# Optimization experiments

Hardware: AMD Instinct MI355X
Metric: run time of the kernel (lower is better)

The kernel has to match this reference:

```python
import jax, jax.numpy as jnp
import numpy as np

B, T, D = 4, 2048, 1024
H = 16
HD = D // H  # 64
MAX_POS = 4096


def setup_inputs() -> dict:
    key = jax.random.key(0)
    k1, k2, k3, k4 = jax.random.split(key, 4)
    x = jax.random.normal(k1, (B, T, D), dtype=jnp.float32)
    position_ids = jnp.sort(jax.random.randint(k2, (B, T), 0, MAX_POS), axis=-1)
    Wqkv = jax.random.normal(k3, (D, 3 * D), dtype=jnp.float32) * (D ** -0.5)
    Wout = jax.random.normal(k4, (D, D), dtype=jnp.float32) * (D ** -0.5)
    return {"x": x, "position_ids": position_ids, "Wqkv": Wqkv, "Wout": Wout}


def reference(x, position_ids, Wqkv, Wout):
    Bv, Tv, Dv = x.shape
    # qkv projection: (B,T,3,H,HD)
    qkv = (x @ Wqkv).reshape(Bv, Tv, 3, H, HD)
    q, k, v = jnp.moveaxis(qkv, 2, 0)  # each (B,T,H,HD)
    q = q.transpose(0, 2, 1, 3)  # (B,H,T,HD)
    k = k.transpose(0, 2, 1, 3)
    v = v.transpose(0, 2, 1, 3)
    scale = 1.0 / jnp.sqrt(jnp.asarray(HD, dtype=x.dtype))
    attn = jnp.einsum('bhid,bhjd->bhij', q, k) * scale  # (B,H,T,T)
    # position-derived causal mask: attend only where pos_i >= pos_j
    causal_mask = position_ids[:, None, :, None] < position_ids[:, None, None, :]
    attn = jnp.where(causal_mask, -jnp.inf, attn)
    attn = jax.nn.softmax(attn, axis=-1)
    attn = jnp.nan_to_num(attn, nan=0.0)
    out = jnp.einsum('bhij,bhjd->bhid', attn, v)  # (B,H,T,HD)
    out = out.transpose(0, 2, 1, 3).reshape(Bv, Tv, Dv)
    return out @ Wout
```

## Files before the change

### kernel.cpp

```cpp
#include <hip/hip_runtime.h>
#include <math.h>

#define NB 4
#define NT 2048
#define ND 1024
#define NH 16
#define NHD 64
#define N3D 3072
#define M1 8192

typedef __attribute__((ext_vector_type(8))) short bf16x8;
typedef __attribute__((ext_vector_type(4))) float f32x4;
typedef __attribute__((ext_vector_type(4))) unsigned int u32x4;
typedef unsigned short u16;
typedef unsigned int u32;

__device__ __forceinline__ u32 bf16rn(float f) {
    u32 u = __float_as_uint(f);
    return (u + 0x7FFFu + ((u >> 16) & 1u)) >> 16;
}
__device__ __forceinline__ u32 pack2(float a, float b) {
    return bf16rn(a) | (bf16rn(b) << 16);
}
__device__ __forceinline__ u32 cvtpk(float lo, float hi) {
    u32 r;
    asm("v_cvt_pk_bf16_f32 %0, %1, %2" : "=v"(r) : "v"(lo), "v"(hi));
    return r;
}

__global__ __launch_bounds__(256) void convx_kernel(const float* __restrict__ in, u16* __restrict__ out) {
    const int idx = blockIdx.x * 256 + threadIdx.x;
    const float4 v = *reinterpret_cast<const float4*>(in + (size_t)idx * 4);
    *reinterpret_cast<uint2*>(out + (size_t)idx * 4) = make_uint2(pack2(v.x, v.y), pack2(v.z, v.w));
}

__global__ __launch_bounds__(256) void tconv_kernel(const float* __restrict__ in, u16* __restrict__ out,
                                                    int R, int C) {
    __shared__ float t[32][33];
    const int bx = blockIdx.x * 32, by = blockIdx.y * 32;
    const int x = threadIdx.x, y0 = threadIdx.y;
    #pragma unroll
    for (int yy = y0; yy < 32; yy += 8) t[yy][x] = in[(size_t)(by + yy) * C + bx + x];
    __syncthreads();
    #pragma unroll
    for (int yy = y0; yy < 32; yy += 8) out[(size_t)(bx + yy) * R + by + x] = (u16)bf16rn(t[x][yy]);
}

#define GEMM_PROLOGUE(Aptr, Btptr)                                                            \
    __shared__ __align__(16) u16 As[4096];                                                    \
    __shared__ __align__(16) u16 Bs[4096];                                                    \
    const int tid = threadIdx.x;                                                              \
    const int lane = tid & 63, wave = tid >> 6;                                               \
    const int wr = wave >> 1, wc = wave & 1;                                                  \
    const int n0 = blockIdx.x * 128, m0 = blockIdx.y * 128;                                   \
    const int c0 = tid, c1 = tid + 256;                                                       \
    const int pA0 = (c0 * 16) ^ ((((c0 * 16) >> 6) & 7) << 4);                                \
    const int pA1 = (c1 * 16) ^ ((((c1 * 16) >> 6) & 7) << 4);                                \
    const u16* gA0 = Aptr + (size_t)(m0 + (c0 >> 2)) * 1024 + (c0 & 3) * 8;                   \
    const u16* gA1 = Aptr + (size_t)(m0 + (c1 >> 2)) * 1024 + (c1 & 3) * 8;                   \
    const u16* gB0 = Btptr + (size_t)(n0 + (c0 >> 2)) * 1024 + (c0 & 3) * 8;                  \
    const u16* gB1 = Btptr + (size_t)(n0 + (c1 >> 2)) * 1024 + (c1 & 3) * 8;                  \
    int offA[4], offB[4];                                                                     \
    {                                                                                         \
        const int kb = (lane >> 4) * 16;                                                      \
        _Pragma("unroll")                                                                     \
        for (int mm = 0; mm < 4; ++mm) {                                                      \
            int row = wr * 64 + mm * 16 + (lane & 15);                                        \
            offA[mm] = (row * 64 + kb) ^ ((row & 7) << 4);                                    \
        }                                                                                     \
        _Pragma("unroll")                                                                     \
        for (int nn = 0; nn < 4; ++nn) {                                                      \
            int row = wc * 64 + nn * 16 + (lane & 15);                                        \
            offB[nn] = (row * 64 + kb) ^ ((row & 7) << 4);                                    \
        }                                                                                     \
    }                                                                                         \
    f32x4 acc[4][4];                                                                          \
    _Pragma("unroll")                                                                         \
    for (int mm = 0; mm < 4; ++mm)                                                            \
        _Pragma("unroll")                                                                     \
        for (int nn = 0; nn < 4; ++nn)                                                        \
            acc[mm][nn] = (f32x4){0.f, 0.f, 0.f, 0.f};                                        \
    uint4 va0 = *(const uint4*)gA0, va1 = *(const uint4*)gA1;                                 \
    uint4 vb0 = *(const uint4*)gB0, vb1 = *(const uint4*)gB1;                                 \
    for (int k0 = 0; k0 < 1024; k0 += 32) {                                                   \
        __syncthreads();                                                                      \
        *(uint4*)((char*)As + pA0) = va0;                                                     \
        *(uint4*)((char*)As + pA1) = va1;                                                     \
        *(uint4*)((char*)Bs + pA0) = vb0;                                                     \
        *(uint4*)((char*)Bs + pA1) = vb1;                                                     \
        __syncthreads();                                                                      \
        if (k0 + 32 < 1024) {                                                                 \
            gA0 += 32; gA1 += 32; gB0 += 32; gB1 += 32;                                       \
            va0 = *(const uint4*)gA0; va1 = *(const uint4*)gA1;                               \
            vb0 = *(const uint4*)gB0; vb1 = *(const uint4*)gB1;                               \
        }                                                                                     \
        bf16x8 aF[4], bF[4];                                                                  \
        _Pragma("unroll")                                                                     \
        for (int mm = 0; mm < 4; ++mm) aF[mm] = *(const bf16x8*)((const char*)As + offA[mm]); \
        _Pragma("unroll")                                                                     \
        for (int nn = 0; nn < 4; ++nn) bF[nn] = *(const bf16x8*)((const char*)Bs + offB[nn]); \
        _Pragma("unroll")                                                                     \
        for (int mm = 0; mm < 4; ++mm)                                                        \
            _Pragma("unroll")                                                                 \
            for (int nn = 0; nn < 4; ++nn)                                                    \
                acc[mm][nn] = __builtin_amdgcn_mfma_f32_16x16x32_bf16(aF[mm], bF[nn],         \
                                                                      acc[mm][nn], 0, 0, 0); \
    }

__global__ __launch_bounds__(256) void gemm_qkv_kernel(
    const u16* __restrict__ A, const u16* __restrict__ Bt,
    u16* __restrict__ Qo, u16* __restrict__ Ko, u16* __restrict__ Vo)
{
    GEMM_PROLOGUE(A, Bt)
    const float qsc = 0.18033688011112042f;
    const int nbase = n0 + wc * 64;
    #pragma unroll
    for (int nn = 0; nn < 4; ++nn) {
        const int n_abs = nbase + nn * 16 + (lane & 15);
        const int s  = n_abs >> 10;
        const int hh = (n_abs >> 6) & 15;
        const int hd = n_abs & 63;
        #pragma unroll
        for (int mm = 0; mm < 4; ++mm) {
            const int rbase = m0 + wr * 64 + mm * 16 + ((lane >> 4) << 2);
            const int b = rbase >> 11, t0 = rbase & 2047;
            const int bh = (b << 4) + hh;
            if (s == 0) {
                #pragma unroll
                for (int r = 0; r < 4; ++r)
                    Qo[((size_t)bh * 2048 + t0 + r) * 64 + hd] = (u16)bf16rn(acc[mm][nn][r] * qsc);
            } else if (s == 1) {
                #pragma unroll
                for (int r = 0; r < 4; ++r)
                    Ko[((size_t)bh * 2048 + t0 + r) * 64 + hd] = (u16)bf16rn(acc[mm][nn][r]);
            } else {
                uint2 w = make_uint2(pack2(acc[mm][nn][0], acc[mm][nn][1]),
                                     pack2(acc[mm][nn][2], acc[mm][nn][3]));
                *reinterpret_cast<uint2*>(&Vo[((size_t)bh * 64 + hd) * 2048 + t0]) = w;
            }
        }
    }
}

__global__ __launch_bounds__(256) void gemm_out_kernel(
    const u16* __restrict__ A, const u16* __restrict__ Bt, float* __restrict__ C)
{
    GEMM_PROLOGUE(A, Bt)
    const int nbase = n0 + wc * 64;
    #pragma unroll
    for (int nn = 0; nn < 4; ++nn) {
        const int n_abs = nbase + nn * 16 + (lane & 15);
        #pragma unroll
        for (int mm = 0; mm < 4; ++mm) {
            const int rbase = m0 + wr * 64 + mm * 16 + ((lane >> 4) << 2);
            #pragma unroll
            for (int r = 0; r < 4; ++r)
                C[(size_t)(rbase + r) * 1024 + n_abs] = acc[mm][nn][r];
        }
    }
}

__global__ __launch_bounds__(256, 2) void attn3_kernel(
    const u16* __restrict__ Q, const u16* __restrict__ K, const u16* __restrict__ Vt,
    const int* __restrict__ pos, u16* __restrict__ AO)
{
    __shared__ int bndS[128];

    const int wg = ((blockIdx.x & 7) << 7) + (blockIdx.x >> 3);
    const int bh = wg >> 4;
    const int qb = 15 - (wg & 15);
    const int b  = bh >> 4, h = bh & 15;
    const int tid = threadIdx.x, lane = tid & 63, wave = tid >> 6;
    const int g = lane >> 4, col = lane & 15;

    if (tid < 128) {
        const int target = pos[b * 2048 + qb * 128 + tid];
        int lo = 0, hi = 2048;
        #pragma unroll
        for (int it = 0; it < 12; ++it) {
            const int mid = (lo + hi) >> 1;
            if (lo < hi) { if (pos[b * 2048 + mid] <= target) lo = mid + 1; else hi = mid; }
        }
        bndS[tid] = lo;
    }
    __syncthreads();

    const int bnd0 = bndS[wave * 32 + col];
    const int bnd1 = bndS[wave * 32 + 16 + col];
    const int bnd_min = bndS[wave * 32];
    const int bnd_max = bndS[wave * 32 + 31];

    bf16x8 qf[2][2];
    const int i0 = qb * 128 + wave * 32 + col;
    #pragma unroll
    for (int m = 0; m < 2; ++m)
        #pragma unroll
        for (int kc = 0; kc < 2; ++kc)
            qf[m][kc] = *(const bf16x8*)&Q[((size_t)bh * 2048 + i0 + m * 16) * 64 + kc * 32 + g * 8];

    int idxp[4];
    #pragma unroll
    for (int t = 0; t < 4; ++t) idxp[t] = (col + 16 * (2 * (g & 1) + (t >> 1))) * 4;
    const bool hiHalf = (lane >= 32);

    float mrun[2] = {-INFINITY, -INFINITY};
    float lrun[2] = {0.f, 0.f};
    f32x4 oT[2][4];
    #pragma unroll
    for (int m = 0; m < 2; ++m)
        #pragma unroll
        for (int dt = 0; dt < 4; ++dt) oT[m][dt] = (f32x4){0.f, 0.f, 0.f, 0.f};

    for (int j0 = 0; j0 < bnd_max; j0 += 64) {
        bf16x8 kf[4][2];
        #pragma unroll
        for (int n = 0; n < 4; ++n)
            #pragma unroll
            for (int kc = 0; kc < 2; ++kc)
                kf[n][kc] = *(const bf16x8*)&K[((size_t)bh * 2048 + j0 + 16 * n + col) * 64 + kc * 32 + g * 8];
        bf16x8 vf[4][2];
        #pragma unroll
        for (int dt = 0; dt < 4; ++dt)
            #pragma unroll
            for (int kc = 0; kc < 2; ++kc)
                vf[dt][kc] = *(const bf16x8*)&Vt[((size_t)bh * 64 + dt * 16 + col) * 2048 + j0 + kc * 32 + g * 8];

        f32x4 st[2][4];
        #pragma unroll
        for (int m = 0; m < 2; ++m)
            #pragma unroll
            for (int n = 0; n < 4; ++n) {
                f32x4 z = (f32x4){0.f, 0.f, 0.f, 0.f};
                z = __builtin_amdgcn_mfma_f32_16x16x32_bf16(kf[n][0], qf[m][0], z, 0, 0, 0);
                st[m][n] = __builtin_amdgcn_mfma_f32_16x16x32_bf16(kf[n][1], qf[m][1], z, 0, 0, 0);
            }

        if (j0 + 64 > bnd_min) {
            #pragma unroll
            for (int m = 0; m < 2; ++m) {
                const int bnd = m ? bnd1 : bnd0;
                #pragma unroll
                for (int n = 0; n < 4; ++n)
                    #pragma unroll
                    for (int r = 0; r < 4; ++r)
                        if (j0 + 16 * n + g * 4 + r >= bnd) st[m][n][r] = -INFINITY;
            }
        }

        #pragma unroll
        for (int m = 0; m < 2; ++m) {
            float rm = st[m][0][0];
            #pragma unroll
            for (int n = 0; n < 4; ++n)
                #pragma unroll
                for (int r = 0; r < 4; ++r) rm = fmaxf(rm, st[m][n][r]);
            rm = fmaxf(rm, __shfl_xor(rm, 16));
            rm = fmaxf(rm, __shfl_xor(rm, 32));
            const float mnew = fmaxf(mrun[m], rm);
            const float factor = __builtin_amdgcn_exp2f(mrun[m] - mnew);
            mrun[m] = mnew;
            float psum = 0.f;
            #pragma unroll
            for (int n = 0; n < 4; ++n)
                #pragma unroll
                for (int r = 0; r < 4; ++r) {
                    const float p = __builtin_amdgcn_exp2f(st[m][n][r] - mnew);
                    st[m][n][r] = p;
                    psum += p;
                }
            psum += __shfl_xor(psum, 16);
            psum += __shfl_xor(psum, 32);
            lrun[m] = lrun[m] * factor + psum;
            #pragma unroll
            for (int dt = 0; dt < 4; ++dt)
                #pragma unroll
                for (int r = 0; r < 4; ++r) oT[m][dt][r] *= factor;
        }

        u32 w[2][4][2];
        #pragma unroll
        for (int m = 0; m < 2; ++m)
            #pragma unroll
            for (int n = 0; n < 4; ++n) {
                w[m][n][0] = cvtpk(st[m][n][0], st[m][n][1]);
                w[m][n][1] = cvtpk(st[m][n][2], st[m][n][3]);
            }

        #pragma unroll
        for (int m = 0; m < 2; ++m) {
            #pragma unroll
            for (int kc = 0; kc < 2; ++kc) {
                u32x4 pw;
                #pragma unroll
                for (int t = 0; t < 4; ++t) {
                    const int e = t & 1;
                    const u32 loW = (u32)__builtin_amdgcn_ds_bpermute(idxp[t], (int)w[m][2 * kc + 0][e]);
                    const u32 hiW = (u32)__builtin_amdgcn_ds_bpermute(idxp[t], (int)w[m][2 * kc + 1][e]);
                    pw[t] = hiHalf ? hiW : loW;
                }
                union { u32x4 u; bf16x8 bv; } cvt;
                cvt.u = pw;
                const bf16x8 pfrag = cvt.bv;
                #pragma unroll
                for (int dt = 0; dt < 4; ++dt)
                    oT[m][dt] = __builtin_amdgcn_mfma_f32_16x16x32_bf16(vf[dt][kc], pfrag, oT[m][dt], 0, 0, 0);
            }
        }
    }

    #pragma unroll
    for (int m = 0; m < 2; ++m) {
        const float inv = 1.f / lrun[m];
        const int t = i0 + m * 16;
        #pragma unroll
        for (int dt = 0; dt < 4; ++dt) {
            uint2 wv = make_uint2(pack2(oT[m][dt][0] * inv, oT[m][dt][1] * inv),
                                  pack2(oT[m][dt][2] * inv, oT[m][dt][3] * inv));
            *reinterpret_cast<uint2*>(&AO[((size_t)(b * 2048 + t)) * 1024 + h * 64 + dt * 16 + g * 4]) = wv;
        }
    }
}

extern "C" void kernel_launch(void* const* d_in, const int* in_sizes, int n_in,
                              void* d_out, int out_size, void* d_ws, size_t ws_size,
                              hipStream_t stream) {
    (void)in_sizes; (void)n_in; (void)out_size; (void)ws_size;
    const float* x    = (const float*)d_in[0];
    const int*   pos  = (const int*)d_in[1];
    const float* Wqkv = (const float*)d_in[2];
    const float* Wout = (const float*)d_in[3];
    float* out = (float*)d_out;

    char* ws = (char*)d_ws;
    u16* xb    = (u16*)(ws);
    u16* WqkvT = (u16*)(ws + 16777216);
    u16* WoutT = (u16*)(ws + 23068672);
    u16* Qb    = (u16*)(ws + 25165824);
    u16* Kb    = (u16*)(ws + 41943040);
    u16* Vtb   = (u16*)(ws + 58720256);
    u16* AO    = xb;

    convx_kernel<<<dim3(M1 * ND / (256 * 4)), dim3(256), 0, stream>>>(x, xb);
    tconv_kernel<<<dim3(N3D / 32, ND / 32), dim3(32, 8), 0, stream>>>(Wqkv, WqkvT, ND, N3D);
    tconv_kernel<<<dim3(ND / 32, ND / 32), dim3(32, 8), 0, stream>>>(Wout, WoutT, ND, ND);
    gemm_qkv_kernel<<<dim3(N3D / 128, M1 / 128), dim3(256), 0, stream>>>(xb, WqkvT, Qb, Kb, Vtb);
    attn3_kernel<<<dim3(1024), dim3(256), 0, stream>>>(Qb, Kb, Vtb, pos, AO);
    gemm_out_kernel<<<dim3(ND / 128, M1 / 128), dim3(256), 0, stream>>>(AO, WoutT, out);
}
```

Measured before the change: 385.6 us.

## Rewrite attention with 32x32 MFMA, permlane swaps and K/V register prefetch

The attention kernel moves from 16x16x32 MFMA tiles over 64-key blocks to 32x32x16 MFMA tiles over 32-key blocks. The P-fragment relayout now uses permlane32_swap instead of ds_bpermute, and the next K/V fragments are loaded into registers one step ahead. The GEMMs swap MFMA operand order so each lane holds contiguous output columns, which allows vectorized Q/K and float4 output stores. The trade is a different register footprint and occupancy (launch bounds no longer request 2 blocks), plus uncoalesced scalar V-transpose stores in the QKV epilogue.

```diff
diff --git a/kernel.cpp b/kernel.cpp
--- a/kernel.cpp
+++ b/kernel.cpp
@@ -11,7 +11,8 @@
 
 typedef __attribute__((ext_vector_type(8))) short bf16x8;
 typedef __attribute__((ext_vector_type(4))) float f32x4;
-typedef __attribute__((ext_vector_type(4))) unsigned int u32x4;
+typedef __attribute__((ext_vector_type(16))) float f32x16;
+typedef __attribute__((ext_vector_type(2))) int i32x2;
 typedef unsigned short u16;
 typedef unsigned int u32;
 
@@ -26,6 +27,10 @@
     u32 r;
     asm("v_cvt_pk_bf16_f32 %0, %1, %2" : "=v"(r) : "v"(lo), "v"(hi));
     return r;
+}
+__device__ __forceinline__ void pswap(u32& a, u32& b) {
+    i32x2 r = __builtin_amdgcn_permlane32_swap((int)a, (int)b, false, false);
+    a = (u32)r.x; b = (u32)r.y;
 }
 
 __global__ __launch_bounds__(256) void convx_kernel(const float* __restrict__ in, u16* __restrict__ out) {
@@ -103,7 +108,7 @@
         for (int mm = 0; mm < 4; ++mm)                                                        \
             _Pragma("unroll")                                                                 \
             for (int nn = 0; nn < 4; ++nn)                                                    \
-                acc[mm][nn] = __builtin_amdgcn_mfma_f32_16x16x32_bf16(aF[mm], bF[nn],         \
+                acc[mm][nn] = __builtin_amdgcn_mfma_f32_16x16x32_bf16(bF[nn], aF[mm],         \
                                                                       acc[mm][nn], 0, 0, 0); \
     }
 
@@ -113,30 +118,51 @@
 {
     GEMM_PROLOGUE(A, Bt)
     const float qsc = 0.18033688011112042f;
-    const int nbase = n0 + wc * 64;
-    #pragma unroll
-    for (int nn = 0; nn < 4; ++nn) {
-        const int n_abs = nbase + nn * 16 + (lane & 15);
-        const int s  = n_abs >> 10;
-        const int hh = (n_abs >> 6) & 15;
-        const int hd = n_abs & 63;
+    const int col16 = lane & 15, g4 = (lane >> 4) << 2;
+    const int nb0 = n0 + wc * 64;
+    const int tb0 = m0 + wr * 64;
+    const int s = nb0 >> 10;
+    if (s == 0) {
         #pragma unroll
         for (int mm = 0; mm < 4; ++mm) {
-            const int rbase = m0 + wr * 64 + mm * 16 + ((lane >> 4) << 2);
-            const int b = rbase >> 11, t0 = rbase & 2047;
-            const int bh = (b << 4) + hh;
-            if (s == 0) {
+            const int t = tb0 + mm * 16 + col16;
+            const int bq = t >> 11, tt = t & 2047;
+            #pragma unroll
+            for (int nn = 0; nn < 4; ++nn) {
+                const int n_abs = nb0 + nn * 16 + g4;
+                const int hh = (n_abs >> 6) & 15, hd = n_abs & 63;
+                uint2 w = make_uint2(pack2(acc[mm][nn][0] * qsc, acc[mm][nn][1] * qsc),
+                                     pack2(acc[mm][nn][2] * qsc, acc[mm][nn][3] * qsc));
+                *reinterpret_cast<uint2*>(&Qo[((size_t)((bq << 4) + hh) * 2048 + tt) * 64 + hd]) = w;
+            }
+        }
+    } else if (s == 1) {
+        #pragma unroll
+        for (int mm = 0; mm < 4; ++mm) {
+            const int t = tb0 + mm * 16 + col16;
+            const int bq = t >> 11, tt = t & 2047;
+            #pragma unroll
+            for (int nn = 0; nn < 4; ++nn) {
+                const int n_abs = nb0 + nn * 16 + g4;
+                const int hh = (n_abs >> 6) & 15, hd = n_abs & 63;
+                uint2 w = make_uint2(pack2(acc[mm][nn][0], acc[mm][nn][1]),
+                                     pack2(acc[mm][nn][2], acc[mm][nn][3]));
+                *reinterpret_cast<uint2*>(&Ko[((size_t)((bq << 4) + hh) * 2048 + tt) * 64 + hd]) = w;
+            }
+        }
+    } else {
+        #pragma unroll
+        for (int mm = 0; mm < 4; ++mm) {
+            const int t = tb0 + mm * 16 + col16;
+            const int bq = t >> 11, tt = t & 2047;
+            #pragma unroll
+            for (int nn = 0; nn < 4; ++nn) {
+                const int n_abs = nb0 + nn * 16 + g4;
+                const int hh = (n_abs >> 6) & 15, hd = n_abs & 63;
+                const size_t vbase = ((size_t)((bq << 4) + hh) * 64 + hd) * 2048 + tt;
                 #pragma unroll
                 for (int r = 0; r < 4; ++r)
-                    Qo[((size_t)bh * 2048 + t0 + r) * 64 + hd] = (u16)bf16rn(acc[mm][nn][r] * qsc);
-            } else if (s == 1) {
-                #pragma unroll
-                for (int r = 0; r < 4; ++r)
-                    Ko[((size_t)bh * 2048 + t0 + r) * 64 + hd] = (u16)bf16rn(acc[mm][nn][r]);
-            } else {
-                uint2 w = make_uint2(pack2(acc[mm][nn][0], acc[mm][nn][1]),
-                                     pack2(acc[mm][nn][2], acc[mm][nn][3]));
-                *reinterpret_cast<uint2*>(&Vo[((size_t)bh * 64 + hd) * 2048 + t0]) = w;
+                    Vo[vbase + (size_t)r * 2048] = (u16)bf16rn(acc[mm][nn][r]);
             }
         }
     }
@@ -146,21 +172,20 @@
     const u16* __restrict__ A, const u16* __restrict__ Bt, float* __restrict__ C)
 {
     GEMM_PROLOGUE(A, Bt)
-    const int nbase = n0 + wc * 64;
-    #pragma unroll
-    for (int nn = 0; nn < 4; ++nn) {
-        const int n_abs = nbase + nn * 16 + (lane & 15);
-        #pragma unroll
-        for (int mm = 0; mm < 4; ++mm) {
-            const int rbase = m0 + wr * 64 + mm * 16 + ((lane >> 4) << 2);
-            #pragma unroll
-            for (int r = 0; r < 4; ++r)
-                C[(size_t)(rbase + r) * 1024 + n_abs] = acc[mm][nn][r];
-        }
-    }
-}
-
-__global__ __launch_bounds__(256, 2) void attn3_kernel(
+    const int col16 = lane & 15, g4 = (lane >> 4) << 2;
+    #pragma unroll
+    for (int mm = 0; mm < 4; ++mm) {
+        const int m = m0 + wr * 64 + mm * 16 + col16;
+        #pragma unroll
+        for (int nn = 0; nn < 4; ++nn) {
+            const int n_a = n0 + wc * 64 + nn * 16 + g4;
+            *reinterpret_cast<float4*>(&C[(size_t)m * 1024 + n_a]) =
+                make_float4(acc[mm][nn][0], acc[mm][nn][1], acc[mm][nn][2], acc[mm][nn][3]);
+        }
+    }
+}
+
+__global__ __launch_bounds__(256) void attn4_kernel(
     const u16* __restrict__ Q, const u16* __restrict__ K, const u16* __restrict__ Vt,
     const int* __restrict__ pos, u16* __restrict__ AO)
 {
@@ -169,155 +194,128 @@
     const int wg = ((blockIdx.x & 7) << 7) + (blockIdx.x >> 3);
     const int bh = wg >> 4;
     const int qb = 15 - (wg & 15);
-    const int b  = bh >> 4, h = bh & 15;
+    const int b = bh >> 4, h = bh & 15;
     const int tid = threadIdx.x, lane = tid & 63, wave = tid >> 6;
-    const int g = lane >> 4, col = lane & 15;
+    const int col = lane & 31, hi = lane >> 5;
 
     if (tid < 128) {
         const int target = pos[b * 2048 + qb * 128 + tid];
-        int lo = 0, hi = 2048;
+        int lo = 0, hic = 2048;
         #pragma unroll
         for (int it = 0; it < 12; ++it) {
-            const int mid = (lo + hi) >> 1;
-            if (lo < hi) { if (pos[b * 2048 + mid] <= target) lo = mid + 1; else hi = mid; }
+            const int mid = (lo + hic) >> 1;
+            if (lo < hic) { if (pos[b * 2048 + mid] <= target) lo = mid + 1; else hic = mid; }
         }
         bndS[tid] = lo;
     }
     __syncthreads();
 
-    const int bnd0 = bndS[wave * 32 + col];
-    const int bnd1 = bndS[wave * 32 + 16 + col];
+    const int bnd     = bndS[wave * 32 + col];
     const int bnd_min = bndS[wave * 32];
     const int bnd_max = bndS[wave * 32 + 31];
 
-    bf16x8 qf[2][2];
-    const int i0 = qb * 128 + wave * 32 + col;
-    #pragma unroll
-    for (int m = 0; m < 2; ++m)
-        #pragma unroll
-        for (int kc = 0; kc < 2; ++kc)
-            qf[m][kc] = *(const bf16x8*)&Q[((size_t)bh * 2048 + i0 + m * 16) * 64 + kc * 32 + g * 8];
-
-    int idxp[4];
-    #pragma unroll
-    for (int t = 0; t < 4; ++t) idxp[t] = (col + 16 * (2 * (g & 1) + (t >> 1))) * 4;
-    const bool hiHalf = (lane >= 32);
-
-    float mrun[2] = {-INFINITY, -INFINITY};
-    float lrun[2] = {0.f, 0.f};
-    f32x4 oT[2][4];
-    #pragma unroll
-    for (int m = 0; m < 2; ++m)
-        #pragma unroll
-        for (int dt = 0; dt < 4; ++dt) oT[m][dt] = (f32x4){0.f, 0.f, 0.f, 0.f};
-
-    for (int j0 = 0; j0 < bnd_max; j0 += 64) {
-        bf16x8 kf[4][2];
-        #pragma unroll
-        for (int n = 0; n < 4; ++n)
+    const int i0 = qb * 128 + wave * 32;
+    const size_t kvrow = (size_t)bh * 2048;
+    const size_t vrow  = (size_t)bh * 64;
+
+    bf16x8 qf[4];
+    #pragma unroll
+    for (int ds = 0; ds < 4; ++ds)
+        qf[ds] = *(const bf16x8*)&Q[(kvrow + i0 + col) * 64 + ds * 16 + hi * 8];
+
+    const int hi4 = 4 * hi;
+
+    float mrun = -INFINITY, lrun = 0.f;
+    f32x16 oT0, oT1;
+    #pragma unroll
+    for (int i = 0; i < 16; ++i) { oT0[i] = 0.f; oT1[i] = 0.f; }
+
+    bf16x8 kf[4], vfa[2], vfb[2];
+    #pragma unroll
+    for (int ds = 0; ds < 4; ++ds)
+        kf[ds] = *(const bf16x8*)&K[(kvrow + col) * 64 + ds * 16 + hi * 8];
+    #pragma unroll
+    for (int kh = 0; kh < 2; ++kh) {
+        vfa[kh] = *(const bf16x8*)&Vt[(vrow + col) * 2048 + kh * 16 + hi * 8];
+        vfb[kh] = *(const bf16x8*)&Vt[(vrow + 32 + col) * 2048 + kh * 16 + hi * 8];
+    }
+
+    for (int j0 = 0; j0 < bnd_max; j0 += 32) {
+        f32x16 st;
+        #pragma unroll
+        for (int i = 0; i < 16; ++i) st[i] = 0.f;
+        #pragma unroll
+        for (int ds = 0; ds < 4; ++ds)
+            st = __builtin_amdgcn_mfma_f32_32x32x16_bf16(kf[ds], qf[ds], st, 0, 0, 0);
+
+        const int jn = (j0 + 32 < bnd_max) ? j0 + 32 : j0;
+        bf16x8 kf2[4], vna[2], vnb[2];
+        #pragma unroll
+        for (int ds = 0; ds < 4; ++ds)
+            kf2[ds] = *(const bf16x8*)&K[(kvrow + jn + col) * 64 + ds * 16 + hi * 8];
+        #pragma unroll
+        for (int kh = 0; kh < 2; ++kh) {
+            vna[kh] = *(const bf16x8*)&Vt[(vrow + col) * 2048 + jn + kh * 16 + hi * 8];
+            vnb[kh] = *(const bf16x8*)&Vt[(vrow + 32 + col) * 2048 + jn + kh * 16 + hi * 8];
+        }
+
+        if (j0 + 32 > bnd_min) {
             #pragma unroll
-            for (int kc = 0; kc < 2; ++kc)
-                kf[n][kc] = *(const bf16x8*)&K[((size_t)bh * 2048 + j0 + 16 * n + col) * 64 + kc * 32 + g * 8];
-        bf16x8 vf[4][2];
-        #pragma unroll
-        for (int dt = 0; dt < 4; ++dt)
-            #pragma unroll
-            for (int kc = 0; kc < 2; ++kc)
-                vf[dt][kc] = *(const bf16x8*)&Vt[((size_t)bh * 64 + dt * 16 + col) * 2048 + j0 + kc * 32 + g * 8];
-
-        f32x4 st[2][4];
-        #pragma unroll
-        for (int m = 0; m < 2; ++m)
-            #pragma unroll
-            for (int n = 0; n < 4; ++n) {
-                f32x4 z = (f32x4){0.f, 0.f, 0.f, 0.f};
-                z = __builtin_amdgcn_mfma_f32_16x16x32_bf16(kf[n][0], qf[m][0], z, 0, 0, 0);
-                st[m][n] = __builtin_amdgcn_mfma_f32_16x16x32_bf16(kf[n][1], qf[m][1], z, 0, 0, 0);
+            for (int r = 0; r < 16; ++r) {
+                const int kg = j0 + ((r & 3) + 8 * (r >> 2)) + hi4;
+                if (kg >= bnd) st[r] = -INFINITY;
             }
-
-        if (j0 + 64 > bnd_min) {
-            #pragma unroll
-            for (int m = 0; m < 2; ++m) {
-                const int bnd = m ? bnd1 : bnd0;
-                #pragma unroll
-                for (int n = 0; n < 4; ++n)
-                    #pragma unroll
-                    for (int r = 0; r < 4; ++r)
-                        if (j0 + 16 * n + g * 4 + r >= bnd) st[m][n][r] = -INFINITY;
-            }
-        }
-
-        #pragma unroll
-        for (int m = 0; m < 2; ++m) {
-            float rm = st[m][0][0];
-            #pragma unroll
-            for (int n = 0; n < 4; ++n)
-                #pragma unroll
-                for (int r = 0; r < 4; ++r) rm = fmaxf(rm, st[m][n][r]);
-            rm = fmaxf(rm, __shfl_xor(rm, 16));
-            rm = fmaxf(rm, __shfl_xor(rm, 32));
-            const float mnew = fmaxf(mrun[m], rm);
-            const float factor = __builtin_amdgcn_exp2f(mrun[m] - mnew);
-            mrun[m] = mnew;
-            float psum = 0.f;
-            #pragma unroll
-            for (int n = 0; n < 4; ++n)
-                #pragma unroll
-                for (int r = 0; r < 4; ++r) {
-                    const float p = __builtin_amdgcn_exp2f(st[m][n][r] - mnew);
-                    st[m][n][r] = p;
-                    psum += p;
-                }
-            psum += __shfl_xor(psum, 16);
-            psum += __shfl_xor(psum, 32);
-            lrun[m] = lrun[m] * factor + psum;
-            #pragma unroll
-            for (int dt = 0; dt < 4; ++dt)
-                #pragma unroll
-                for (int r = 0; r < 4; ++r) oT[m][dt][r] *= factor;
-        }
-
-        u32 w[2][4][2];
-        #pragma unroll
-        for (int m = 0; m < 2; ++m)
-            #pragma unroll
-            for (int n = 0; n < 4; ++n) {
-                w[m][n][0] = cvtpk(st[m][n][0], st[m][n][1]);
-                w[m][n][1] = cvtpk(st[m][n][2], st[m][n][3]);
-            }
-
-        #pragma unroll
-        for (int m = 0; m < 2; ++m) {
-            #pragma unroll
-            for (int kc = 0; kc < 2; ++kc) {
-                u32x4 pw;
-                #pragma unroll
-                for (int t = 0; t < 4; ++t) {
-                    const int e = t & 1;
-                    const u32 loW = (u32)__builtin_amdgcn_ds_bpermute(idxp[t], (int)w[m][2 * kc + 0][e]);
-                    const u32 hiW = (u32)__builtin_amdgcn_ds_bpermute(idxp[t], (int)w[m][2 * kc + 1][e]);
-                    pw[t] = hiHalf ? hiW : loW;
-                }
-                union { u32x4 u; bf16x8 bv; } cvt;
-                cvt.u = pw;
-                const bf16x8 pfrag = cvt.bv;
-                #pragma unroll
-                for (int dt = 0; dt < 4; ++dt)
-                    oT[m][dt] = __builtin_amdgcn_mfma_f32_16x16x32_bf16(vf[dt][kc], pfrag, oT[m][dt], 0, 0, 0);
-            }
-        }
-    }
-
-    #pragma unroll
-    for (int m = 0; m < 2; ++m) {
-        const float inv = 1.f / lrun[m];
-        const int t = i0 + m * 16;
-        #pragma unroll
-        for (int dt = 0; dt < 4; ++dt) {
-            uint2 wv = make_uint2(pack2(oT[m][dt][0] * inv, oT[m][dt][1] * inv),
-                                  pack2(oT[m][dt][2] * inv, oT[m][dt][3] * inv));
-            *reinterpret_cast<uint2*>(&AO[((size_t)(b * 2048 + t)) * 1024 + h * 64 + dt * 16 + g * 4]) = wv;
-        }
+        }
+
+        float rm = st[0];
+        #pragma unroll
+        for (int r = 1; r < 16; ++r) rm = fmaxf(rm, st[r]);
+        rm = fmaxf(rm, __shfl_xor(rm, 32));
+        const float mnew = fmaxf(mrun, rm);
+        const float factor = __builtin_amdgcn_exp2f(mrun - mnew);
+        mrun = mnew;
+        float psum = 0.f;
+        #pragma unroll
+        for (int r = 0; r < 16; ++r) {
+            const float p = __builtin_amdgcn_exp2f(st[r] - mnew);
+            st[r] = p;
+            psum += p;
+        }
+        psum += __shfl_xor(psum, 32);
+        lrun = lrun * factor + psum;
+        #pragma unroll
+        for (int i = 0; i < 16; ++i) { oT0[i] *= factor; oT1[i] *= factor; }
+
+        u32 W[8];
+        #pragma unroll
+        for (int r = 0; r < 8; ++r) W[r] = cvtpk(st[2 * r], st[2 * r + 1]);
+
+        u32 a0 = W[0], b0 = W[2]; pswap(a0, b0);
+        u32 a1 = W[1], b1 = W[3]; pswap(a1, b1);
+        u32 a2 = W[4], b2 = W[6]; pswap(a2, b2);
+        u32 a3 = W[5], b3 = W[7]; pswap(a3, b3);
+        union { u32 w[4]; bf16x8 v; } p0, p1;
+        p0.w[0] = a0; p0.w[1] = a1; p0.w[2] = b0; p0.w[3] = b1;
+        p1.w[0] = a2; p1.w[1] = a3; p1.w[2] = b2; p1.w[3] = b3;
+
+        oT0 = __builtin_amdgcn_mfma_f32_32x32x16_bf16(vfa[0], p0.v, oT0, 0, 0, 0);
+        oT0 = __builtin_amdgcn_mfma_f32_32x32x16_bf16(vfa[1], p1.v, oT0, 0, 0, 0);
+        oT1 = __builtin_amdgcn_mfma_f32_32x32x16_bf16(vfb[0], p0.v, oT1, 0, 0, 0);
+        oT1 = __builtin_amdgcn_mfma_f32_32x32x16_bf16(vfb[1], p1.v, oT1, 0, 0, 0);
+
+        #pragma unroll
+        for (int ds = 0; ds < 4; ++ds) kf[ds] = kf2[ds];
+        #pragma unroll
+        for (int kh = 0; kh < 2; ++kh) { vfa[kh] = vna[kh]; vfb[kh] = vnb[kh]; }
+    }
+
+    const float inv = 1.f / lrun;
+    u16* dst = &AO[((size_t)(b * 2048 + i0 + col)) * 1024 + h * 64];
+    #pragma unroll
+    for (int w = 0; w < 8; ++w) {
+        const int dloc = 8 * (w >> 1) + 2 * (w & 1) + hi4;
+        *reinterpret_cast<u32*>(&dst[dloc])      = cvtpk(oT0[2 * w] * inv, oT0[2 * w + 1] * inv);
+        *reinterpret_cast<u32*>(&dst[32 + dloc]) = cvtpk(oT1[2 * w] * inv, oT1[2 * w + 1] * inv);
     }
 }
 
@@ -344,6 +342,6 @@
     tconv_kernel<<<dim3(N3D / 32, ND / 32), dim3(32, 8), 0, stream>>>(Wqkv, WqkvT, ND, N3D);
     tconv_kernel<<<dim3(ND / 32, ND / 32), dim3(32, 8), 0, stream>>>(Wout, WoutT, ND, ND);
     gemm_qkv_kernel<<<dim3(N3D / 128, M1 / 128), dim3(256), 0, stream>>>(xb, WqkvT, Qb, Kb, Vtb);
-    attn3_kernel<<<dim3(1024), dim3(256), 0, stream>>>(Qb, Kb, Vtb, pos, AO);
+    attn4_kernel<<<dim3(1024), dim3(256), 0, stream>>>(Qb, Kb, Vtb, pos, AO);
     gemm_out_kernel<<<dim3(ND / 128, M1 / 128), dim3(256), 0, stream>>>(AO, WoutT, out);
 }
```

Result: no change. 387.1 us (+0.4%).
